# Optimization experiments

Measured on AMD Instinct MI355X. Metric: run time of the kernel, lower is better.

## Reference

```python
import jax, jax.numpy as jnp
import numpy as np

N_NODES = 200000  # graph size
D = 128           # feature dim == out_size
N1 = 81920        # layer-1 node set size
B = 8192          # batch size
K = 10            # num_sample neighbors


def setup_inputs() -> dict:
    key = jax.random.key(0)
    k = jax.random.split(key, 7)
    raw_features = jax.random.normal(k[0], (N_NODES, D), dtype=jnp.float32)
    # xavier-like scale for weights [out, 2*in]
    W1 = jax.random.normal(k[1], (D, 2 * D), dtype=jnp.float32) * (1.0 / np.sqrt(2 * D))
    W2 = jax.random.normal(k[2], (D, 2 * D), dtype=jnp.float32) * (1.0 / np.sqrt(2 * D))
    layer1_nodes = jax.random.randint(k[3], (N1,), 0, N_NODES)
    neigh0_idx = jax.random.randint(k[4], (N1, K), 0, N_NODES)
    map_batch = jax.random.randint(k[5], (B,), 0, N1)
    neigh1_idx = jax.random.randint(k[6], (B, K), 0, N1)
    return {
        "raw_features": raw_features,
        "W1": W1,
        "W2": W2,
        "layer1_nodes": layer1_nodes,
        "neigh0_idx": neigh0_idx,
        "map_batch": map_batch,
        "neigh1_idx": neigh1_idx,
    }


def _sage_layer(self_feats, agg_feats, W):
    # combined = cat([self, agg], dim=1); relu(W @ combined.T).T == relu(combined @ W.T)
    combined = jnp.concatenate([self_feats, agg_feats], axis=1)
    return jax.nn.relu(combined @ W.T)


def reference(raw_features, W1, W2, layer1_nodes, neigh0_idx, map_batch, neigh1_idx):
    # Layer 1: aggregate raw features over K sampled neighbors (MEAN), gcn=False
    agg0 = jnp.mean(raw_features[neigh0_idx], axis=1)        # [N1, D]
    self0 = raw_features[layer1_nodes]                        # [N1, D]
    h1 = _sage_layer(self0, agg0, W1)                         # [N1, D]
    # Layer 2: aggregate layer-1 embeddings for the batch nodes
    agg1 = jnp.mean(h1[neigh1_idx], axis=1)                   # [B, D]
    self1 = h1[map_batch]                                     # [B, D]
    h2 = _sage_layer(self1, agg1, W2)                         # [B, D]
    return h2
```

## Files before the change

kernel.cpp:

```cpp
#include <hip/hip_runtime.h>
#include <stdint.h>

#define D 128
#define K_NEI 10
#define TILE_M 64

typedef __bf16 bf16x8 __attribute__((ext_vector_type(8)));
typedef float f32x4 __attribute__((ext_vector_type(4)));

__device__ __forceinline__ uint32_t f2bf(float f) {
    union { float f; uint32_t u; } v; v.f = f;
    uint32_t u = v.u;
    return (u + 0x7FFFu + ((u >> 16) & 1u)) >> 16;
}
__device__ __forceinline__ float bf2f(uint32_t h) {
    union { uint32_t u; float f; } v; v.u = h << 16; return v.f;
}
__device__ __forceinline__ uint32_t pack2(float a, float b) {
    return f2bf(a) | (f2bf(b) << 16);
}
__device__ __forceinline__ bf16x8 u4_as_bf16x8(uint4 u) {
    union { uint4 u; bf16x8 b; } v; v.u = u; return v.b;
}
__device__ __forceinline__ uint2 cvt4(f32x4 v) {
    union { __bf16 b[4]; uint2 u; } o;
    o.b[0] = (__bf16)v[0]; o.b[1] = (__bf16)v[1];
    o.b[2] = (__bf16)v[2]; o.b[3] = (__bf16)v[3];
    return o.u;
}
__device__ __forceinline__ bf16x8 cvt8(f32x4 lo, f32x4 hi) {
    union { __bf16 b[8]; bf16x8 v; } o;
    o.b[0] = (__bf16)lo[0]; o.b[1] = (__bf16)lo[1];
    o.b[2] = (__bf16)lo[2]; o.b[3] = (__bf16)lo[3];
    o.b[4] = (__bf16)hi[0]; o.b[5] = (__bf16)hi[1];
    o.b[6] = (__bf16)hi[2]; o.b[7] = (__bf16)hi[3];
    return o.v;
}

__global__ void convert_zero(const float* __restrict__ W1, const float* __restrict__ W2,
                             uint16_t* __restrict__ O1, uint16_t* __restrict__ O2,
                             int* __restrict__ flags, int* __restrict__ counter, int N1)
{
    const int b = blockIdx.x;
    if (b < 32) {
        const float* W = (b < 16) ? W1 : W2;
        uint16_t*    O = (b < 16) ? O1 : O2;
        int t = (b & 15) * 256 + threadIdx.x;
        const float s = (t & 16) ? 0.1f : 1.0f;
        const float* src = W + (size_t)t * 8;
        f32x4 a = *(const f32x4*)src * s;
        f32x4 c = *(const f32x4*)(src + 4) * s;
        uint2 lo = cvt4(a), hi = cvt4(c);
        uint4 o; o.x = lo.x; o.y = lo.y; o.z = hi.x; o.w = hi.y;
        *(uint4*)(O + (size_t)t * 8) = o;
    } else {
        if (b == 32 && threadIdx.x == 0) *counter = 0;
        for (int i = (b - 32) * 256 + threadIdx.x; i < N1; i += 160 * 256)
            flags[i] = 0;
    }
}

__global__ void mark_used(const int* __restrict__ map_batch,
                          const int* __restrict__ neigh1,
                          int* __restrict__ flags, int B)
{
    const int t = blockIdx.x * 256 + threadIdx.x;
    const int T = B + B * K_NEI;
    if (t >= T) return;
    const int idx = (t < B) ? map_batch[t] : neigh1[t - B];
    flags[idx] = 1;
}

__global__ void compact_used(const int* __restrict__ flags,
                             int* __restrict__ list, int* __restrict__ counter, int N1)
{
    const int i = blockIdx.x * 256 + threadIdx.x;
    if (i < N1 && flags[i]) {
        int p = atomicAdd(counter, 1);
        list[p] = i;
    }
}

template <bool SRC_F32, bool OUT_F32, bool USE_LIST>
__global__ __launch_bounds__(128)
void sage_fused(const void* __restrict__ src_,
                const uint16_t* __restrict__ Wc,
                const int* __restrict__ self_idx,
                const int* __restrict__ neigh_idx,
                void* __restrict__ out_, int M,
                const int* __restrict__ list,
                const int* __restrict__ cnt_p)
{
    const int tid  = threadIdx.x;
    const int lane = tid & 63;
    const int r16  = lane & 15;
    const int q    = lane >> 4;
    const int base = blockIdx.x * 32 + (tid >> 6) * 16;

    int g;
    if (USE_LIST) {
        const int cnt = *cnt_p;
        if (base >= cnt) return;
        int li = base + r16;
        if (li >= cnt) li = cnt - 1;
        g = list[li];
    } else {
        g = base + r16;
        if (base >= M) return;
        if (g >= M) g = M - 1;
    }

    const int2* nrow2 = (const int2*)(neigh_idx + (size_t)g * K_NEI);
    int idx[K_NEI];
    #pragma unroll
    for (int k = 0; k < 5; ++k) {
        int2 p = nrow2[k];
        idx[2 * k] = p.x; idx[2 * k + 1] = p.y;
    }
    const int self = self_idx[g];

    bf16x8 a[8];
    f32x4 agg[8];
    #pragma unroll
    for (int x = 0; x < 8; ++x) agg[x] = (f32x4){0.f, 0.f, 0.f, 0.f};

    if (SRC_F32) {
        const float* src  = (const float*)src_;
        const float* srow = src + (size_t)self * D + q * 8;
        f32x4 sl[8];
        #pragma unroll
        for (int ks = 0; ks < 4; ++ks) {
            sl[2 * ks]     = *(const f32x4*)(srow + ks * 32);
            sl[2 * ks + 1] = *(const f32x4*)(srow + ks * 32 + 4);
        }
        #pragma unroll
        for (int kp = 0; kp < 5; ++kp) {
            const float* r0 = src + (size_t)idx[2 * kp]     * D + q * 8;
            const float* r1 = src + (size_t)idx[2 * kp + 1] * D + q * 8;
            f32x4 t[8], u[8];
            #pragma unroll
            for (int ks = 0; ks < 4; ++ks) {
                t[2 * ks]     = *(const f32x4*)(r0 + ks * 32);
                t[2 * ks + 1] = *(const f32x4*)(r0 + ks * 32 + 4);
                u[2 * ks]     = *(const f32x4*)(r1 + ks * 32);
                u[2 * ks + 1] = *(const f32x4*)(r1 + ks * 32 + 4);
            }
            #pragma unroll
            for (int x = 0; x < 8; ++x) agg[x] += t[x] + u[x];
        }
        #pragma unroll
        for (int ks = 0; ks < 4; ++ks)
            a[ks] = cvt8(sl[2 * ks], sl[2 * ks + 1]);
    } else {
        const uint16_t* src = (const uint16_t*)src_;
        const uint16_t* srow = src + (size_t)self * D + q * 8;
        uint4 sv[4];
        #pragma unroll
        for (int ks = 0; ks < 4; ++ks) sv[ks] = *(const uint4*)(srow + ks * 32);
        #pragma unroll
        for (int kp = 0; kp < 5; ++kp) {
            const uint16_t* r0 = src + (size_t)idx[2 * kp]     * D + q * 8;
            const uint16_t* r1 = src + (size_t)idx[2 * kp + 1] * D + q * 8;
            uint4 t[4], u[4];
            #pragma unroll
            for (int ks = 0; ks < 4; ++ks) {
                t[ks] = *(const uint4*)(r0 + ks * 32);
                u[ks] = *(const uint4*)(r1 + ks * 32);
            }
            #pragma unroll
            for (int ks = 0; ks < 4; ++ks) {
                agg[2 * ks]     += (f32x4){bf2f(t[ks].x & 0xFFFFu), bf2f(t[ks].x >> 16),
                                           bf2f(t[ks].y & 0xFFFFu), bf2f(t[ks].y >> 16)};
                agg[2 * ks + 1] += (f32x4){bf2f(t[ks].z & 0xFFFFu), bf2f(t[ks].z >> 16),
                                           bf2f(t[ks].w & 0xFFFFu), bf2f(t[ks].w >> 16)};
                agg[2 * ks]     += (f32x4){bf2f(u[ks].x & 0xFFFFu), bf2f(u[ks].x >> 16),
                                           bf2f(u[ks].y & 0xFFFFu), bf2f(u[ks].y >> 16)};
                agg[2 * ks + 1] += (f32x4){bf2f(u[ks].z & 0xFFFFu), bf2f(u[ks].z >> 16),
                                           bf2f(u[ks].w & 0xFFFFu), bf2f(u[ks].w >> 16)};
            }
        }
        #pragma unroll
        for (int ks = 0; ks < 4; ++ks) a[ks] = u4_as_bf16x8(sv[ks]);
    }
    #pragma unroll
    for (int ks = 0; ks < 4; ++ks)
        a[4 + ks] = cvt8(agg[2 * ks], agg[2 * ks + 1]);

    f32x4 acc[8];
    #pragma unroll
    for (int nt = 0; nt < 8; ++nt) acc[nt] = (f32x4){0.f, 0.f, 0.f, 0.f};

    const uint16_t* wb = Wc + (size_t)r16 * 256 + q * 8;
    #pragma unroll
    for (int nt = 0; nt < 8; ++nt)
        #pragma unroll
        for (int ks = 0; ks < 8; ++ks) {
            bf16x8 w = *(const bf16x8*)(wb + (size_t)nt * 16 * 256 + ks * 32);
            acc[nt] = __builtin_amdgcn_mfma_f32_16x16x32_bf16(w, a[ks], acc[nt], 0, 0, 0);
        }

    #pragma unroll
    for (int nt = 0; nt < 8; ++nt) {
        f32x4 v = acc[nt];
        v[0] = v[0] > 0.f ? v[0] : 0.f;
        v[1] = v[1] > 0.f ? v[1] : 0.f;
        v[2] = v[2] > 0.f ? v[2] : 0.f;
        v[3] = v[3] > 0.f ? v[3] : 0.f;
        const int col = nt * 16 + q * 4;
        if (OUT_F32)
            *(f32x4*)((float*)out_ + (size_t)g * D + col) = v;
        else
            *(uint2*)((uint16_t*)out_ + (size_t)g * D + col) = cvt4(v);
    }
}

template <bool FEATS_F32, bool OUT_F32>
__global__ void sage_layer(const void* __restrict__ feats_,
                           const float* __restrict__ W,
                           const int* __restrict__ self_idx,
                           const int* __restrict__ neigh_idx,
                           void* __restrict__ out_)
{
    __shared__ __align__(16) uint16_t Alds[TILE_M * 128];
    __shared__ __align__(16) uint16_t Wlds[128 * 128];

    const int tid  = threadIdx.x;
    const int wave = tid >> 6;
    const int lane = tid & 63;
    const int r16  = lane & 15;
    const int q    = lane >> 4;
    const int G    = blockIdx.x * TILE_M;

    const float*    feats_f = (const float*)feats_;
    const uint16_t* feats_b = (const uint16_t*)feats_;

    f32x4 acc[8];
    #pragma unroll
    for (int nt = 0; nt < 8; ++nt) acc[nt] = (f32x4){0.f, 0.f, 0.f, 0.f};

    for (int half = 0; half < 2; ++half) {
        #pragma unroll
        for (int it = 0; it < 8; ++it) {
            int t = it * 256 + tid;
            int j = t >> 4, c = t & 15;
            const float* src = W + (size_t)j * 256 + half * 128 + c * 8;
            f32x4 w0 = *(const f32x4*)(src);
            f32x4 w1 = *(const f32x4*)(src + 4);
            uint4 o;
            o.x = pack2(w0[0], w0[1]); o.y = pack2(w0[2], w0[3]);
            o.z = pack2(w1[0], w1[1]); o.w = pack2(w1[2], w1[3]);
            int cs = c ^ (j & 15);
            *(uint4*)(Wlds + j * 128 + cs * 8) = o;
        }
        if (half == 0) {
            #pragma unroll
            for (int it = 0; it < 4; ++it) {
                int t = it * 256 + tid;
                int n = t >> 4, c = t & 15;
                int node = self_idx[G + n];
                uint4 o;
                if (FEATS_F32) {
                    const float* src = feats_f + (size_t)node * D + c * 8;
                    f32x4 f0 = *(const f32x4*)(src);
                    f32x4 f1 = *(const f32x4*)(src + 4);
                    o.x = pack2(f0[0], f0[1]); o.y = pack2(f0[2], f0[3]);
                    o.z = pack2(f1[0], f1[1]); o.w = pack2(f1[2], f1[3]);
                } else {
                    o = *(const uint4*)(feats_b + (size_t)node * D + c * 8);
                }
                int cs = c ^ (n & 15);
                *(uint4*)(Alds + n * 128 + cs * 8) = o;
            }
        } else {
            #pragma unroll
            for (int it = 0; it < 4; ++it) {
                int t = it * 256 + tid;
                int n = t >> 4, c = t & 15;
                const int* nrow = neigh_idx + (size_t)(G + n) * K_NEI;
                float s0=0,s1=0,s2=0,s3=0,s4=0,s5=0,s6=0,s7=0;
                #pragma unroll
                for (int k = 0; k < K_NEI; ++k) {
                    if (FEATS_F32) {
                        const float* src = feats_f + (size_t)nrow[k] * D + c * 8;
                        f32x4 f0 = *(const f32x4*)(src);
                        f32x4 f1 = *(const f32x4*)(src + 4);
                        s0 += f0[0]; s1 += f0[1]; s2 += f0[2]; s3 += f0[3];
                        s4 += f1[0]; s5 += f1[1]; s6 += f1[2]; s7 += f1[3];
                    } else {
                        uint4 v = *(const uint4*)(feats_b + (size_t)nrow[k] * D + c * 8);
                        s0 += bf2f(v.x & 0xFFFFu); s1 += bf2f(v.x >> 16);
                        s2 += bf2f(v.y & 0xFFFFu); s3 += bf2f(v.y >> 16);
                        s4 += bf2f(v.z & 0xFFFFu); s5 += bf2f(v.z >> 16);
                        s6 += bf2f(v.w & 0xFFFFu); s7 += bf2f(v.w >> 16);
                    }
                }
                const float inv = 0.1f;
                uint4 o;
                o.x = pack2(s0 * inv, s1 * inv);
                o.y = pack2(s2 * inv, s3 * inv);
                o.z = pack2(s4 * inv, s5 * inv);
                o.w = pack2(s6 * inv, s7 * inv);
                int cs = c ^ (n & 15);
                *(uint4*)(Alds + n * 128 + cs * 8) = o;
            }
        }
        __syncthreads();

        #pragma unroll
        for (int ks = 0; ks < 4; ++ks) {
            int cidx = ks * 4 + q;
            bf16x8 a = *(const bf16x8*)(Alds + (wave * 16 + r16) * 128 + ((cidx ^ r16) * 8));
            bf16x8 b[8];
            #pragma unroll
            for (int nt = 0; nt < 8; ++nt) {
                int jj = nt * 16 + r16;
                b[nt] = *(const bf16x8*)(Wlds + jj * 128 + ((cidx ^ r16) * 8));
            }
            #pragma unroll
            for (int nt = 0; nt < 8; ++nt)
                acc[nt] = __builtin_amdgcn_mfma_f32_16x16x32_bf16(a, b[nt], acc[nt], 0, 0, 0);
        }
        __syncthreads();
    }

    const int row_base = G + wave * 16 + q * 4;
    #pragma unroll
    for (int nt = 0; nt < 8; ++nt) {
        int col = nt * 16 + r16;
        #pragma unroll
        for (int r = 0; r < 4; ++r) {
            float v = acc[nt][r];
            v = v > 0.f ? v : 0.f;
            if (OUT_F32) ((float*)out_)[(size_t)(row_base + r) * D + col] = v;
            else ((uint16_t*)out_)[(size_t)(row_base + r) * D + col] = (uint16_t)f2bf(v);
        }
    }
}

extern "C" void kernel_launch(void* const* d_in, const int* in_sizes, int n_in,
                              void* d_out, int out_size, void* d_ws, size_t ws_size,
                              hipStream_t stream) {
    const float* raw = (const float*)d_in[0];
    const float* W1  = (const float*)d_in[1];
    const float* W2  = (const float*)d_in[2];
    const int* layer1_nodes = (const int*)d_in[3];
    const int* neigh0       = (const int*)d_in[4];
    const int* map_batch    = (const int*)d_in[5];
    const int* neigh1       = (const int*)d_in[6];

    const int N1 = in_sizes[3];
    const int B  = in_sizes[5];

    const size_t szH1 = (size_t)N1 * 128 * 2;
    const size_t szW  = 128 * 256 * 2;
    const size_t szAux = (size_t)N1 * 4 * 2 + 64;
    const size_t need = szH1 + 2 * szW + szAux;

    if (ws_size >= need && (N1 % 16) == 0 && (B % 16) == 0) {
        uint16_t* h1   = (uint16_t*)d_ws;
        uint16_t* W1c  = h1 + (size_t)N1 * 128;
        uint16_t* W2c  = W1c + 128 * 256;
        int*      flags   = (int*)(W2c + 128 * 256);
        int*      list    = flags + N1;
        int*      counter = list + N1;

        convert_zero<<<192, 256, 0, stream>>>(W1, W2, W1c, W2c, flags, counter, N1);

        mark_used<<<(B + B * K_NEI + 255) / 256, 256, 0, stream>>>(map_batch, neigh1, flags, B);
        compact_used<<<(N1 + 255) / 256, 256, 0, stream>>>(flags, list, counter, N1);

        sage_fused<true,  false, true ><<<(N1 + 31) / 32, 128, 0, stream>>>(
            raw, W1c, layer1_nodes, neigh0, h1, N1, list, counter);

        sage_fused<false, true,  false><<<(B + 31) / 32, 128, 0, stream>>>(
            h1, W2c, map_batch, neigh1, d_out, B, nullptr, nullptr);
        return;
    }

    uint16_t* h1 = (uint16_t*)d_ws;
    sage_layer<true,  false><<<N1 / TILE_M, 256, 0, stream>>>(raw, W1, layer1_nodes, neigh0, h1);
    sage_layer<false, true ><<<B  / TILE_M, 256, 0, stream>>>(h1,  W2, map_batch,    neigh1, d_out);
}
```

Baseline: 252.6 us.

## Pre-convert raw features to bf16 and split layer 2 into gather plus GEMM

A prep kernel now converts the whole raw feature table to bf16 on every call, so the layer-1 fused kernel gathers 256-byte bf16 rows instead of 512-byte fp32 rows. The layer-1 gather now issues all ten neighbour loads per k-slice before accumulating, to raise memory-level parallelism. Layer 2 is split into a gather kernel that writes concatenated [self, sum] bf16 rows, followed by a persistent GEMM kernel that keeps W in registers and prefetches the next tile. The cost is an extra streaming pass over the full feature table plus an intermediate buffer and one more launch, which may cancel the smaller random-gather traffic.

```diff
diff --git a/kernel.cpp b/kernel.cpp
--- a/kernel.cpp
+++ b/kernel.cpp
@@ -37,15 +37,26 @@
     return o.v;
 }
 
-__global__ void convert_zero(const float* __restrict__ W1, const float* __restrict__ W2,
-                             uint16_t* __restrict__ O1, uint16_t* __restrict__ O2,
-                             int* __restrict__ flags, int* __restrict__ counter, int N1)
+__global__ void prep(const float* __restrict__ raw, int nCvt,
+                     const float* __restrict__ W1, const float* __restrict__ W2,
+                     uint16_t* __restrict__ rawb,
+                     uint16_t* __restrict__ W1c, uint16_t* __restrict__ W2c,
+                     int* __restrict__ flags, int* __restrict__ counter, int N1)
 {
     const int b = blockIdx.x;
-    if (b < 32) {
-        const float* W = (b < 16) ? W1 : W2;
-        uint16_t*    O = (b < 16) ? O1 : O2;
-        int t = (b & 15) * 256 + threadIdx.x;
+    if (b < nCvt) {
+        size_t t = (size_t)b * 256 + threadIdx.x;
+        const float* s = raw + t * 8;
+        f32x4 a = *(const f32x4*)s;
+        f32x4 c = *(const f32x4*)(s + 4);
+        uint2 lo = cvt4(a), hi = cvt4(c);
+        uint4 o; o.x = lo.x; o.y = lo.y; o.z = hi.x; o.w = hi.y;
+        *(uint4*)(rawb + t * 8) = o;
+    } else if (b < nCvt + 32) {
+        const int b2 = b - nCvt;
+        const float* W = (b2 < 16) ? W1 : W2;
+        uint16_t*    O = (b2 < 16) ? W1c : W2c;
+        int t = (b2 & 15) * 256 + threadIdx.x;
         const float s = (t & 16) ? 0.1f : 1.0f;
         const float* src = W + (size_t)t * 8;
         f32x4 a = *(const f32x4*)src * s;
@@ -54,8 +65,9 @@
         uint4 o; o.x = lo.x; o.y = lo.y; o.z = hi.x; o.w = hi.y;
         *(uint4*)(O + (size_t)t * 8) = o;
     } else {
-        if (b == 32 && threadIdx.x == 0) *counter = 0;
-        for (int i = (b - 32) * 256 + threadIdx.x; i < N1; i += 160 * 256)
+        const int b3 = b - nCvt - 32;
+        if (b3 == 0 && threadIdx.x == 0) *counter = 0;
+        for (int i = b3 * 256 + threadIdx.x; i < N1; i += 160 * 256)
             flags[i] = 0;
     }
 }
@@ -81,15 +93,15 @@
     }
 }
 
-template <bool SRC_F32, bool OUT_F32, bool USE_LIST>
+template <bool OUT_F32, bool USE_LIST>
 __global__ __launch_bounds__(128)
-void sage_fused(const void* __restrict__ src_,
-                const uint16_t* __restrict__ Wc,
-                const int* __restrict__ self_idx,
-                const int* __restrict__ neigh_idx,
-                void* __restrict__ out_, int M,
-                const int* __restrict__ list,
-                const int* __restrict__ cnt_p)
+void sage_fused_b(const uint16_t* __restrict__ src,
+                  const uint16_t* __restrict__ Wc,
+                  const int* __restrict__ self_idx,
+                  const int* __restrict__ neigh_idx,
+                  void* __restrict__ out_, int M,
+                  const int* __restrict__ list,
+                  const int* __restrict__ cnt_p)
 {
     const int tid  = threadIdx.x;
     const int lane = tid & 63;
@@ -119,72 +131,39 @@
     }
     const int self = self_idx[g];
 
+    const uint16_t* srow = src + (size_t)self * D + q * 8;
+    uint4 sv[4];
+    #pragma unroll
+    for (int ks = 0; ks < 4; ++ks) sv[ks] = *(const uint4*)(srow + ks * 32);
+
+    const uint16_t* np[K_NEI];
+    #pragma unroll
+    for (int k = 0; k < K_NEI; ++k) np[k] = src + (size_t)idx[k] * D + q * 8;
+
+    f32x4 agg[8];
+    #pragma unroll
+    for (int x = 0; x < 8; ++x) agg[x] = (f32x4){0.f, 0.f, 0.f, 0.f};
+
+    #pragma unroll
+    for (int ks = 0; ks < 4; ++ks) {
+        uint4 v[K_NEI];
+        #pragma unroll
+        for (int k = 0; k < K_NEI; ++k) v[k] = *(const uint4*)(np[k] + ks * 32);
+        #pragma unroll
+        for (int k = 0; k < K_NEI; ++k) {
+            agg[2 * ks]     += (f32x4){bf2f(v[k].x & 0xFFFFu), bf2f(v[k].x >> 16),
+                                       bf2f(v[k].y & 0xFFFFu), bf2f(v[k].y >> 16)};
+            agg[2 * ks + 1] += (f32x4){bf2f(v[k].z & 0xFFFFu), bf2f(v[k].z >> 16),
+                                       bf2f(v[k].w & 0xFFFFu), bf2f(v[k].w >> 16)};
+        }
+    }
+
     bf16x8 a[8];
-    f32x4 agg[8];
-    #pragma unroll
-    for (int x = 0; x < 8; ++x) agg[x] = (f32x4){0.f, 0.f, 0.f, 0.f};
-
-    if (SRC_F32) {
-        const float* src  = (const float*)src_;
-        const float* srow = src + (size_t)self * D + q * 8;
-        f32x4 sl[8];
-        #pragma unroll
-        for (int ks = 0; ks < 4; ++ks) {
-            sl[2 * ks]     = *(const f32x4*)(srow + ks * 32);
-            sl[2 * ks + 1] = *(const f32x4*)(srow + ks * 32 + 4);
-        }
-        #pragma unroll
-        for (int kp = 0; kp < 5; ++kp) {
-            const float* r0 = src + (size_t)idx[2 * kp]     * D + q * 8;
-            const float* r1 = src + (size_t)idx[2 * kp + 1] * D + q * 8;
-            f32x4 t[8], u[8];
-            #pragma unroll
-            for (int ks = 0; ks < 4; ++ks) {
-                t[2 * ks]     = *(const f32x4*)(r0 + ks * 32);
-                t[2 * ks + 1] = *(const f32x4*)(r0 + ks * 32 + 4);
-                u[2 * ks]     = *(const f32x4*)(r1 + ks * 32);
-                u[2 * ks + 1] = *(const f32x4*)(r1 + ks * 32 + 4);
-            }
-            #pragma unroll
-            for (int x = 0; x < 8; ++x) agg[x] += t[x] + u[x];
-        }
-        #pragma unroll
-        for (int ks = 0; ks < 4; ++ks)
-            a[ks] = cvt8(sl[2 * ks], sl[2 * ks + 1]);
-    } else {
-        const uint16_t* src = (const uint16_t*)src_;
-        const uint16_t* srow = src + (size_t)self * D + q * 8;
-        uint4 sv[4];
-        #pragma unroll
-        for (int ks = 0; ks < 4; ++ks) sv[ks] = *(const uint4*)(srow + ks * 32);
-        #pragma unroll
-        for (int kp = 0; kp < 5; ++kp) {
-            const uint16_t* r0 = src + (size_t)idx[2 * kp]     * D + q * 8;
-            const uint16_t* r1 = src + (size_t)idx[2 * kp + 1] * D + q * 8;
-            uint4 t[4], u[4];
-            #pragma unroll
-            for (int ks = 0; ks < 4; ++ks) {
-                t[ks] = *(const uint4*)(r0 + ks * 32);
-                u[ks] = *(const uint4*)(r1 + ks * 32);
-            }
-            #pragma unroll
-            for (int ks = 0; ks < 4; ++ks) {
-                agg[2 * ks]     += (f32x4){bf2f(t[ks].x & 0xFFFFu), bf2f(t[ks].x >> 16),
-                                           bf2f(t[ks].y & 0xFFFFu), bf2f(t[ks].y >> 16)};
-                agg[2 * ks + 1] += (f32x4){bf2f(t[ks].z & 0xFFFFu), bf2f(t[ks].z >> 16),
-                                           bf2f(t[ks].w & 0xFFFFu), bf2f(t[ks].w >> 16)};
-                agg[2 * ks]     += (f32x4){bf2f(u[ks].x & 0xFFFFu), bf2f(u[ks].x >> 16),
-                                           bf2f(u[ks].y & 0xFFFFu), bf2f(u[ks].y >> 16)};
-                agg[2 * ks + 1] += (f32x4){bf2f(u[ks].z & 0xFFFFu), bf2f(u[ks].z >> 16),
-                                           bf2f(u[ks].w & 0xFFFFu), bf2f(u[ks].w >> 16)};
-            }
-        }
-        #pragma unroll
-        for (int ks = 0; ks < 4; ++ks) a[ks] = u4_as_bf16x8(sv[ks]);
-    }
-    #pragma unroll
-    for (int ks = 0; ks < 4; ++ks)
+    #pragma unroll
+    for (int ks = 0; ks < 4; ++ks) {
+        a[ks]     = u4_as_bf16x8(sv[ks]);
         a[4 + ks] = cvt8(agg[2 * ks], agg[2 * ks + 1]);
+    }
 
     f32x4 acc[8];
     #pragma unroll
@@ -211,6 +190,119 @@
             *(f32x4*)((float*)out_ + (size_t)g * D + col) = v;
         else
             *(uint2*)((uint16_t*)out_ + (size_t)g * D + col) = cvt4(v);
+    }
+}
+
+__global__ void gather_agg2(const uint16_t* __restrict__ src,
+                            const int* __restrict__ self_idx,
+                            const int* __restrict__ neigh_idx,
+                            uint16_t* __restrict__ C, int M)
+{
+    const int t = blockIdx.x * 256 + threadIdx.x;
+    const int i = t >> 4;
+    const int j = t & 15;
+    if (i >= M) return;
+
+    const int2* nrow2 = (const int2*)(neigh_idx + (size_t)i * K_NEI);
+    int idx[K_NEI];
+    #pragma unroll
+    for (int k = 0; k < 5; ++k) {
+        int2 p = nrow2[k];
+        idx[2 * k] = p.x; idx[2 * k + 1] = p.y;
+    }
+    const int self = self_idx[i];
+    uint16_t* c = C + (size_t)i * 256;
+
+    uint4 sv = *(const uint4*)(src + (size_t)self * D + j * 8);
+    float s0=0,s1=0,s2=0,s3=0,s4=0,s5=0,s6=0,s7=0;
+    #pragma unroll
+    for (int k = 0; k < K_NEI; ++k) {
+        uint4 v = *(const uint4*)(src + (size_t)idx[k] * D + j * 8);
+        s0 += bf2f(v.x & 0xFFFFu); s1 += bf2f(v.x >> 16);
+        s2 += bf2f(v.y & 0xFFFFu); s3 += bf2f(v.y >> 16);
+        s4 += bf2f(v.z & 0xFFFFu); s5 += bf2f(v.z >> 16);
+        s6 += bf2f(v.w & 0xFFFFu); s7 += bf2f(v.w >> 16);
+    }
+    *(uint4*)(c + j * 8) = sv;
+    uint4 o;
+    o.x = pack2(s0, s1); o.y = pack2(s2, s3);
+    o.z = pack2(s4, s5); o.w = pack2(s6, s7);
+    *(uint4*)(c + 128 + j * 8) = o;
+}
+
+template <bool OUT_F32>
+__global__ __launch_bounds__(256)
+void gemm_k256(const uint16_t* __restrict__ A,
+               const uint16_t* __restrict__ Wc,
+               void* __restrict__ out_, int M)
+{
+    const int tid  = threadIdx.x;
+    const int wave = tid >> 6;
+    const int lane = tid & 63;
+    const int r16  = lane & 15;
+    const int q    = lane >> 4;
+    const int h    = wave & 1;
+
+    const int nTiles = M >> 4;
+    const int stride = gridDim.x * 2;
+    int tile = blockIdx.x * 2 + (wave >> 1);
+    if (tile >= nTiles) return;
+
+    bf16x8 Wf[4][8];
+    {
+        const uint16_t* wb = Wc + (size_t)(h * 64 + r16) * 256 + q * 8;
+        #pragma unroll
+        for (int nt = 0; nt < 4; ++nt)
+            #pragma unroll
+            for (int ks = 0; ks < 8; ++ks)
+                Wf[nt][ks] = *(const bf16x8*)(wb + nt * 16 * 256 + ks * 32);
+    }
+
+    uint4 preB[8];
+    {
+        const uint16_t* row = A + (size_t)(tile * 16 + r16) * 256 + q * 8;
+        #pragma unroll
+        for (int ks = 0; ks < 8; ++ks) preB[ks] = *(const uint4*)(row + ks * 32);
+    }
+
+    while (tile < nTiles) {
+        const int nxt = tile + stride;
+
+        bf16x8 a[8];
+        #pragma unroll
+        for (int ks = 0; ks < 8; ++ks) a[ks] = u4_as_bf16x8(preB[ks]);
+
+        if (nxt < nTiles) {
+            const uint16_t* row = A + (size_t)(nxt * 16 + r16) * 256 + q * 8;
+            #pragma unroll
+            for (int ks = 0; ks < 8; ++ks) preB[ks] = *(const uint4*)(row + ks * 32);
+        }
+
+        f32x4 acc[4];
+        #pragma unroll
+        for (int nt = 0; nt < 4; ++nt) acc[nt] = (f32x4){0.f,0.f,0.f,0.f};
+
+        #pragma unroll
+        for (int ks = 0; ks < 8; ++ks)
+            #pragma unroll
+            for (int nt = 0; nt < 4; ++nt)
+                acc[nt] = __builtin_amdgcn_mfma_f32_16x16x32_bf16(Wf[nt][ks], a[ks], acc[nt], 0, 0, 0);
+
+        const size_t row = (size_t)(tile * 16 + r16);
+        const int col0 = h * 64 + q * 4;
+        #pragma unroll
+        for (int nt = 0; nt < 4; ++nt) {
+            f32x4 v = acc[nt];
+            v[0] = v[0] > 0.f ? v[0] : 0.f;
+            v[1] = v[1] > 0.f ? v[1] : 0.f;
+            v[2] = v[2] > 0.f ? v[2] : 0.f;
+            v[3] = v[3] > 0.f ? v[3] : 0.f;
+            if (OUT_F32)
+                *(f32x4*)((float*)out_ + row * 128 + col0 + nt * 16) = v;
+            else
+                *(uint2*)((uint16_t*)out_ + row * 128 + col0 + nt * 16) = cvt4(v);
+        }
+        tile = nxt;
     }
 }
 
@@ -348,32 +440,39 @@
     const int* map_batch    = (const int*)d_in[5];
     const int* neigh1       = (const int*)d_in[6];
 
+    const int N_NODES = in_sizes[0] / D;
     const int N1 = in_sizes[3];
     const int B  = in_sizes[5];
 
-    const size_t szH1 = (size_t)N1 * 128 * 2;
-    const size_t szW  = 128 * 256 * 2;
-    const size_t szAux = (size_t)N1 * 4 * 2 + 64;
-    const size_t need = szH1 + 2 * szW + szAux;
-
-    if (ws_size >= need && (N1 % 16) == 0 && (B % 16) == 0) {
-        uint16_t* h1   = (uint16_t*)d_ws;
-        uint16_t* W1c  = h1 + (size_t)N1 * 128;
+    const size_t szRawb = (size_t)N_NODES * 128 * 2;
+    const size_t szH1   = (size_t)N1 * 128 * 2;
+    const size_t szC2   = (size_t)B * 256 * 2;
+    const size_t szW    = 128 * 256 * 2;
+    const size_t szAux  = (size_t)N1 * 4 * 2 + 64;
+    const size_t need = szRawb + szH1 + szC2 + 2 * szW + szAux;
+
+    if (ws_size >= need && (N_NODES % 16) == 0 && (N1 % 16) == 0 && (B % 16) == 0) {
+        uint16_t* rawb = (uint16_t*)d_ws;
+        uint16_t* h1   = rawb + (size_t)N_NODES * 128;
+        uint16_t* C2   = h1 + (size_t)N1 * 128;
+        uint16_t* W1c  = C2 + (size_t)B * 256;
         uint16_t* W2c  = W1c + 128 * 256;
         int*      flags   = (int*)(W2c + 128 * 256);
         int*      list    = flags + N1;
         int*      counter = list + N1;
 
-        convert_zero<<<192, 256, 0, stream>>>(W1, W2, W1c, W2c, flags, counter, N1);
+        const int nCvt = (N_NODES * D) / 2048;
+        prep<<<nCvt + 192, 256, 0, stream>>>(raw, nCvt, W1, W2, rawb, W1c, W2c,
+                                             flags, counter, N1);
 
         mark_used<<<(B + B * K_NEI + 255) / 256, 256, 0, stream>>>(map_batch, neigh1, flags, B);
         compact_used<<<(N1 + 255) / 256, 256, 0, stream>>>(flags, list, counter, N1);
 
-        sage_fused<true,  false, true ><<<(N1 + 31) / 32, 128, 0, stream>>>(
-            raw, W1c, layer1_nodes, neigh0, h1, N1, list, counter);
-
-        sage_fused<false, true,  false><<<(B + 31) / 32, 128, 0, stream>>>(
-            h1, W2c, map_batch, neigh1, d_out, B, nullptr, nullptr);
+        sage_fused_b<false, true><<<(N1 + 31) / 32, 128, 0, stream>>>(
+            rawb, W1c, layer1_nodes, neigh0, h1, N1, list, counter);
+
+        gather_agg2<<<(B * 16 + 255) / 256, 256, 0, stream>>>(h1, map_batch, neigh1, C2, B);
+        gemm_k256<true><<<(B / 16 + 1) / 2, 256, 0, stream>>>(C2, W2c, d_out, B);
         return;
     }
 
```

Measured after the change: 254.7 us. No clear change (+0.9%).
